# Optimization experiments

Measured on AMD Instinct MI355X. Metric: run time of the kernel, lower is better.

The kernel has to match this reference:

```python
import jax, jax.numpy as jnp
import numpy as np

N_NODES = 50000
N_EDGES = 800000
IN_F, HID, NCLS = 128, 64, 64
N_EXTRA = 2          # layer - 2
K_STEPS = 10
ALPHA = 0.1
BN_EPS = 1e-5


def setup_inputs() -> dict:
    key = jax.random.key(0)
    ks = jax.random.split(key, 20)
    d = {}
    d['x'] = jax.random.normal(ks[0], (N_NODES, IN_F), dtype=jnp.float32)
    d['edge_index'] = jax.random.randint(ks[1], (2, N_EDGES), 0, N_NODES, dtype=jnp.int64)
    s = 1.0 / np.sqrt(HID)
    d['W1'] = jax.random.normal(ks[2], (IN_F, HID), dtype=jnp.float32) / np.sqrt(IN_F)
    d['b1'] = jnp.zeros((HID,), jnp.float32)
    d['W2'] = jax.random.normal(ks[3], (HID, HID), dtype=jnp.float32) * s
    d['b2'] = jnp.zeros((HID,), jnp.float32)
    d['Wx'] = jax.random.normal(ks[4], (N_EXTRA, HID, HID), dtype=jnp.float32) * s
    d['bx'] = jnp.zeros((N_EXTRA, HID), jnp.float32)
    d['g1'] = jnp.ones((HID,), jnp.float32); d['be1'] = jnp.zeros((HID,), jnp.float32)
    d['g2'] = jnp.ones((HID,), jnp.float32); d['be2'] = jnp.zeros((HID,), jnp.float32)
    d['g3'] = jnp.ones((HID,), jnp.float32); d['be3'] = jnp.zeros((HID,), jnp.float32)
    d['Wfc'] = jax.random.normal(ks[5], (HID, NCLS), dtype=jnp.float32) * s
    d['bfc'] = jnp.zeros((NCLS,), jnp.float32)
    return d


def _gcn_norm(edge_index, n):
    # add self-loops, symmetric D^-1/2 (A+I) D^-1/2 normalization (PyG GCNConv default)
    loop = jnp.arange(n, dtype=edge_index.dtype)
    src = jnp.concatenate([edge_index[0], loop])
    dst = jnp.concatenate([edge_index[1], loop])
    deg = jax.ops.segment_sum(jnp.ones(src.shape[0], jnp.float32), dst, num_segments=n)
    dinv = jnp.where(deg > 0, jax.lax.rsqrt(deg), 0.0)
    return src, dst, dinv[src] * dinv[dst]


def _propagate(x, src, dst, w, n):
    # gather-scale-scatter: out[dst] += w * x[src]
    return jax.ops.segment_sum(x[src] * w[:, None], dst, num_segments=n)


def _bn(x, g, b):
    # BatchNorm1d in training mode: batch statistics over the node dim
    m = jnp.mean(x, axis=0)
    v = jnp.var(x, axis=0)
    return g * (x - m) * jax.lax.rsqrt(v + BN_EPS) + b


def reference(x, edge_index, W1, b1, W2, b2, Wx, bx, g1, be1, g2, be2, g3, be3, Wfc, bfc):
    n = x.shape[0]
    src, dst, w = _gcn_norm(edge_index, n)
    h = _propagate(x @ W1, src, dst, w, n) + b1
    h = jax.nn.relu(_bn(h, g1, be1))
    h = _propagate(h @ W2, src, dst, w, n) + b2
    h = jax.nn.relu(_bn(h, g2, be2))
    for i in range(Wx.shape[0]):
        h = _propagate(h @ Wx[i], src, dst, w, n) + bx[i]
        h = jax.nn.relu(_bn(h, g3, be3))
    # APPNP: K power-iteration steps with teleport back to h0
    h0 = h
    for _ in range(K_STEPS):
        h = (1.0 - ALPHA) * _propagate(h, src, dst, w, n) + ALPHA * h0
    out = h @ Wfc + bfc
    return jax.nn.log_softmax(out, axis=1)
```

## Files before the change

### kernel.cpp

```cpp
#include <hip/hip_runtime.h>
#include <hip/hip_fp16.h>
#include <cstdint>
#include <cstddef>

#define NN 50000
#define NE 800000
#define HID 64
#define INF_ 128
#define BN_EPS 1e-5f
#define NGRP (NN / 8)
#define NG16 (NN / 16)
#define SCAN_B 196
#define NSLICE 32

typedef float floatx2 __attribute__((ext_vector_type(2)));

__device__ __forceinline__ float4 h8_to_f4(float2 raw) {
    union { float f; __half2 h; } ua, ub;
    ua.f = raw.x; ub.f = raw.y;
    float2 fa = __half22float2(ua.h), fb = __half22float2(ub.h);
    return make_float4(fa.x, fa.y, fb.x, fb.y);
}
__device__ __forceinline__ float2 f4_to_h8(float4 v) {
    union { float f; __half2 h; } ua, ub;
    ua.h = __float22half2_rn(make_float2(v.x, v.y));
    ub.h = __float22half2_rn(make_float2(v.z, v.w));
    return make_float2(ua.f, ub.f);
}
struct f8 { float v[8]; };
__device__ __forceinline__ f8 h16_to_f8(float4 raw) {
    f8 r;
    union { float f; __half2 h; } u;
    float2 a;
    u.f = raw.x; a = __half22float2(u.h); r.v[0] = a.x; r.v[1] = a.y;
    u.f = raw.y; a = __half22float2(u.h); r.v[2] = a.x; r.v[3] = a.y;
    u.f = raw.z; a = __half22float2(u.h); r.v[4] = a.x; r.v[5] = a.y;
    u.f = raw.w; a = __half22float2(u.h); r.v[6] = a.x; r.v[7] = a.y;
    return r;
}
__device__ __forceinline__ float4 f8_to_h16(const f8& s) {
    union { float f; __half2 h; } u;
    float4 o;
    u.h = __float22half2_rn(make_float2(s.v[0], s.v[1])); o.x = u.f;
    u.h = __float22half2_rn(make_float2(s.v[2], s.v[3])); o.y = u.f;
    u.h = __float22half2_rn(make_float2(s.v[4], s.v[5])); o.z = u.f;
    u.h = __float22half2_rn(make_float2(s.v[6], s.v[7])); o.w = u.f;
    return o;
}

__device__ __forceinline__ void fp8x8_to_f(unsigned lo, unsigned hi, float out[8]) {
    floatx2 a = __builtin_amdgcn_cvt_pk_f32_fp8((int)lo, false);
    floatx2 b = __builtin_amdgcn_cvt_pk_f32_fp8((int)lo, true);
    floatx2 c = __builtin_amdgcn_cvt_pk_f32_fp8((int)hi, false);
    floatx2 d = __builtin_amdgcn_cvt_pk_f32_fp8((int)hi, true);
    out[0] = a[0]; out[1] = a[1]; out[2] = b[0]; out[3] = b[1];
    out[4] = c[0]; out[5] = c[1]; out[6] = d[0]; out[7] = d[1];
}
__device__ __forceinline__ void fp8x16_to_f(uint4 r, float out[16]) {
    fp8x8_to_f(r.x, r.y, out);
    fp8x8_to_f(r.z, r.w, out + 8);
}
__device__ __forceinline__ uint2 f_to_fp8x8(const float v[8]) {
    int w0 = __builtin_amdgcn_cvt_pk_fp8_f32(v[0], v[1], 0, false);
    w0 = __builtin_amdgcn_cvt_pk_fp8_f32(v[2], v[3], w0, true);
    int w1 = __builtin_amdgcn_cvt_pk_fp8_f32(v[4], v[5], 0, false);
    w1 = __builtin_amdgcn_cvt_pk_fp8_f32(v[6], v[7], w1, true);
    uint2 o; o.x = (unsigned)w0; o.y = (unsigned)w1;
    return o;
}
__device__ __forceinline__ uint4 f_to_fp8x16(const float v[16]) {
    uint2 a = f_to_fp8x8(v), b = f_to_fp8x8(v + 8);
    uint4 o; o.x = a.x; o.y = a.y; o.z = b.x; o.w = b.y;
    return o;
}


__global__ void count_k(const int* __restrict__ dst, int* __restrict__ cnt) {
    int e = blockIdx.x * blockDim.x + threadIdx.x;
    if (e < NE) atomicAdd(&cnt[dst[e]], 1);
}

__global__ void dinv_k(const int* __restrict__ cnt, float* __restrict__ dinv) {
    int n = blockIdx.x * blockDim.x + threadIdx.x;
    if (n < NN) dinv[n] = rsqrtf((float)(cnt[n] + 1));
}

__global__ void scan1_k(const int* __restrict__ cnt, int* __restrict__ offs,
                        int* __restrict__ bsum) {
    __shared__ int sh[256];
    int t = threadIdx.x, i = blockIdx.x * 256 + t;
    int v = (i < NN) ? ((cnt[i] + 7) & ~7) : 0;
    sh[t] = v;
    __syncthreads();
    for (int d = 1; d < 256; d <<= 1) {
        int u = (t >= d) ? sh[t - d] : 0;
        __syncthreads();
        sh[t] += u;
        __syncthreads();
    }
    if (i < NN) offs[i] = sh[t] - v;
    if (t == 255) bsum[blockIdx.x] = sh[255];
}

__global__ void scan2_k(const int* __restrict__ bsum, int* __restrict__ bpre,
                        int* __restrict__ offs) {
    __shared__ int sh[256];
    int t = threadIdx.x;
    int v = (t < SCAN_B) ? bsum[t] : 0;
    sh[t] = v;
    __syncthreads();
    for (int d = 1; d < 256; d <<= 1) {
        int u = (t >= d) ? sh[t - d] : 0;
        __syncthreads();
        sh[t] += u;
        __syncthreads();
    }
    bpre[t] = sh[t] - v;
    if (t == 255) offs[NN] = sh[255];
}

__global__ void scan3_k(int* __restrict__ offs, const int* __restrict__ bpre) {
    int i = blockIdx.x * blockDim.x + threadIdx.x;
    if (i < NN) offs[i] += bpre[i >> 8];
}

__global__ void pad_k(const int* __restrict__ cnt, const int* __restrict__ offs,
                      int2* __restrict__ edge2) {
    int n = blockIdx.x * blockDim.x + threadIdx.x;
    if (n >= NN) return;
    int e = offs[n] + cnt[n], e1 = offs[n + 1];
    for (; e < e1; ++e) edge2[e] = make_int2(0, 0);
}

__global__ void scatter_k(const int* __restrict__ src, const int* __restrict__ dst,
                          const int* __restrict__ offs, int* __restrict__ cursor,
                          const float* __restrict__ dinv,
                          int2* __restrict__ edge2) {
    int e = blockIdx.x * blockDim.x + threadIdx.x;
    if (e < NE) {
        int s = src[e], d = dst[e];
        int pos = offs[d] + atomicAdd(&cursor[d], 1);
        edge2[pos] = make_int2(s, __float_as_int(dinv[s] * dinv[d]));
    }
}

template <int K, bool HIN>
__global__ __launch_bounds__(256, 2) void mm_k(const void* __restrict__ Xv,
                                               const float* __restrict__ W,
                                               float2* __restrict__ Y) {
    constexpr int RS = K + 4;
    __shared__ float Xs[64 * RS];
    __shared__ float Ws[K * 64];
    const int t = threadIdx.x;
    const int n0 = blockIdx.x * 64;

    {
        const float4* Wg = (const float4*)W;
        for (int g2 = t; g2 < K * 16; g2 += 256) {
            int row = g2 >> 4, c4 = g2 & 15;
            *(float4*)&Ws[row * 64 + c4 * 4] = Wg[g2];
        }
    }
    if (HIN) {
        const float4* Xg = (const float4*)Xv;
        for (int g2 = t; g2 < 64 * (K / 8); g2 += 256) {
            int row = g2 / (K / 8), c8 = g2 % (K / 8);
            int rr = n0 + row; if (rr >= NN) rr = NN - 1;
            f8 v = h16_to_f8(Xg[(size_t)rr * (K / 8) + c8]);
            float* dp = &Xs[row * RS + c8 * 8];
#pragma unroll
            for (int j = 0; j < 8; ++j) dp[j] = v.v[j];
        }
    } else {
        const float4* Xg = (const float4*)Xv;
        for (int g2 = t; g2 < 64 * (K / 4); g2 += 256) {
            int row = g2 / (K / 4), c4 = g2 % (K / 4);
            int rr = n0 + row; if (rr >= NN) rr = NN - 1;
            *(float4*)&Xs[row * RS + c4 * 4] = Xg[(size_t)rr * (K / 4) + c4];
        }
    }
    __syncthreads();

    const int r0 = (t >> 4) << 2;
    const int c0 = (t & 15) << 2;
    float acc[4][4];
#pragma unroll
    for (int j = 0; j < 4; ++j)
#pragma unroll
        for (int c = 0; c < 4; ++c) acc[j][c] = 0.f;

#pragma unroll 8
    for (int kq = 0; kq < K / 4; ++kq) {
        float4 xv[4];
#pragma unroll
        for (int j = 0; j < 4; ++j)
            xv[j] = *(const float4*)&Xs[(r0 + j) * RS + kq * 4];
        float4 wv[4];
#pragma unroll
        for (int i = 0; i < 4; ++i)
            wv[i] = *(const float4*)&Ws[(kq * 4 + i) * 64 + c0];
#pragma unroll
        for (int j = 0; j < 4; ++j) {
            acc[j][0] = fmaf(xv[j].x, wv[0].x, acc[j][0]);
            acc[j][1] = fmaf(xv[j].x, wv[0].y, acc[j][1]);
            acc[j][2] = fmaf(xv[j].x, wv[0].z, acc[j][2]);
            acc[j][3] = fmaf(xv[j].x, wv[0].w, acc[j][3]);
            acc[j][0] = fmaf(xv[j].y, wv[1].x, acc[j][0]);
            acc[j][1] = fmaf(xv[j].y, wv[1].y, acc[j][1]);
            acc[j][2] = fmaf(xv[j].y, wv[1].z, acc[j][2]);
            acc[j][3] = fmaf(xv[j].y, wv[1].w, acc[j][3]);
            acc[j][0] = fmaf(xv[j].z, wv[2].x, acc[j][0]);
            acc[j][1] = fmaf(xv[j].z, wv[2].y, acc[j][1]);
            acc[j][2] = fmaf(xv[j].z, wv[2].z, acc[j][2]);
            acc[j][3] = fmaf(xv[j].z, wv[2].w, acc[j][3]);
            acc[j][0] = fmaf(xv[j].w, wv[3].x, acc[j][0]);
            acc[j][1] = fmaf(xv[j].w, wv[3].y, acc[j][1]);
            acc[j][2] = fmaf(xv[j].w, wv[3].z, acc[j][2]);
            acc[j][3] = fmaf(xv[j].w, wv[3].w, acc[j][3]);
        }
    }

#pragma unroll
    for (int j = 0; j < 4; ++j) {
        int rr = n0 + r0 + j;
        if (rr < NN)
            Y[(size_t)rr * 16 + (t & 15)] =
                f4_to_h8(make_float4(acc[j][0], acc[j][1], acc[j][2], acc[j][3]));
    }
}

__device__ __forceinline__ void prop_gather8(const float4* __restrict__ X4,
                                             const int2* __restrict__ E,
                                             int e0, int e1, int fl, int slotbase,
                                             float acc[8], float acc2[8]) {
    if (e0 >= e1) return;
    int2 d0 = E[e0 + fl];
    int srcs[8]; float ws[8];
#pragma unroll
    for (int i = 0; i < 8; ++i) {
        srcs[i] = __shfl(d0.x, slotbase + i, 64);
        ws[i]   = __shfl(__int_as_float(d0.y), slotbase + i, 64);
    }
    int2 d1;
    if (e0 + 8 < e1) d1 = E[e0 + 8 + fl];
    float4 rr[8];
#pragma unroll
    for (int i = 0; i < 8; ++i) rr[i] = X4[(size_t)srcs[i] * 8 + fl];

    for (int e = e0; e < e1; ) {
        int en = e + 8;
        float4 rn[8]; float wn[8];
        if (en < e1) {
            int sn[8];
#pragma unroll
            for (int i = 0; i < 8; ++i) {
                sn[i] = __shfl(d1.x, slotbase + i, 64);
                wn[i] = __shfl(__int_as_float(d1.y), slotbase + i, 64);
            }
            if (en + 8 < e1) d1 = E[en + 8 + fl];
#pragma unroll
            for (int i = 0; i < 8; ++i) rn[i] = X4[(size_t)sn[i] * 8 + fl];
        }
        __builtin_amdgcn_sched_barrier(0);
#pragma unroll
        for (int i = 0; i < 8; ++i) {
            f8 x = h16_to_f8(rr[i]);
            float* a = (i & 1) ? acc2 : acc;
#pragma unroll
            for (int j = 0; j < 8; ++j)
                a[j] = fmaf(ws[i], x.v[j], a[j]);
        }
        e = en;
        if (e < e1) {
#pragma unroll
            for (int i = 0; i < 8; ++i) { rr[i] = rn[i]; ws[i] = wn[i]; }
        }
    }
}

__global__ __launch_bounds__(256, 2) void prop_stats_k(
        const float4* __restrict__ X4, const int* __restrict__ offs,
        const int2* __restrict__ edge2, const float* __restrict__ dinv,
        const float* __restrict__ bias, float4* __restrict__ Y4,
        float* __restrict__ stats) {
    const int lane = threadIdx.x & 63;
    const int wave = threadIdx.x >> 6;
    const int slot = lane >> 3;
    const int fl = lane & 7;
    const int slotbase = lane & 56;
    const int wid = blockIdx.x * 4 + wave;
    const int nw = gridDim.x * 4;

    float bias8[8];
    {
        float4 b0 = ((const float4*)bias)[fl * 2];
        float4 b1 = ((const float4*)bias)[fl * 2 + 1];
        bias8[0] = b0.x; bias8[1] = b0.y; bias8[2] = b0.z; bias8[3] = b0.w;
        bias8[4] = b1.x; bias8[5] = b1.y; bias8[6] = b1.z; bias8[7] = b1.w;
    }

    float s1[8], s2[8];
#pragma unroll
    for (int j = 0; j < 8; ++j) { s1[j] = 0.f; s2[j] = 0.f; }

    for (int g = wid; g < NGRP; g += nw) {
        int n = g * 8 + slot;
        float dn = dinv[n];
        float dd = dn * dn;
        f8 self = h16_to_f8(X4[(size_t)n * 8 + fl]);
        float acc[8], acc2[8];
#pragma unroll
        for (int j = 0; j < 8; ++j) { acc[j] = dd * self.v[j]; acc2[j] = 0.f; }
        int e0 = offs[n], e1 = offs[n + 1];
        prop_gather8(X4, edge2, e0, e1, fl, slotbase, acc, acc2);
        f8 o;
#pragma unroll
        for (int j = 0; j < 8; ++j) {
            float a = acc[j] + acc2[j] + bias8[j];
            o.v[j] = a;
            s1[j] += a;
            s2[j] = fmaf(a, a, s2[j]);
        }
        Y4[(size_t)n * 8 + fl] = f8_to_h16(o);
    }

#pragma unroll
    for (int m = 8; m <= 32; m <<= 1) {
#pragma unroll
        for (int j = 0; j < 8; ++j) {
            s1[j] += __shfl_xor(s1[j], m, 64);
            s2[j] += __shfl_xor(s2[j], m, 64);
        }
    }

    __shared__ float red[4][8][16];
    if (lane < 8) {
#pragma unroll
        for (int j = 0; j < 8; ++j) {
            red[wave][lane][j] = s1[j];
            red[wave][lane][8 + j] = s2[j];
        }
    }
    __syncthreads();
    int t = threadIdx.x;
    if (t < 128) {
        int j = t & 63;
        int isq = t >> 6;
        int fli = j >> 3, c = (j & 7) + isq * 8;
        float a = red[0][fli][c] + red[1][fli][c] + red[2][fli][c] + red[3][fli][c];
        atomicAdd(&stats[(blockIdx.x & (NSLICE - 1)) * 128 + isq * 64 + j], a);
    }
}

__global__ __launch_bounds__(256) void bn_relu_k(
        const float4* __restrict__ Y4, const float* __restrict__ slices,
        const float* __restrict__ g, const float* __restrict__ be,
        float4* __restrict__ H4) {
    __shared__ float fs[128];
    int t = threadIdx.x;
    if (t < 128) {
        float s = 0.f;
#pragma unroll
        for (int k = 0; k < NSLICE; ++k) s += slices[k * 128 + t];
        fs[t] = s;
    }
    __syncthreads();
    int i = blockIdx.x * blockDim.x + t;
    if (i >= NN * 8) return;
    int fg = i & 7;
    const float invN = 1.f / (float)NN;
    f8 y = h16_to_f8(Y4[i]);
    float4 gv0 = ((const float4*)g)[fg * 2];
    float4 gv1 = ((const float4*)g)[fg * 2 + 1];
    float4 bv0 = ((const float4*)be)[fg * 2];
    float4 bv1 = ((const float4*)be)[fg * 2 + 1];
    float gv[8] = { gv0.x, gv0.y, gv0.z, gv0.w, gv1.x, gv1.y, gv1.z, gv1.w };
    float bv[8] = { bv0.x, bv0.y, bv0.z, bv0.w, bv1.x, bv1.y, bv1.z, bv1.w };
    f8 o;
#pragma unroll
    for (int j = 0; j < 8; ++j) {
        float m = fs[fg * 8 + j] * invN;
        float v = fs[64 + fg * 8 + j] * invN - m * m;
        float val = fmaf(gv[j] * rsqrtf(v + BN_EPS), y.v[j] - m, bv[j]);
        o.v[j] = val > 0.f ? val : 0.f;
    }
    H4[i] = f8_to_h16(o);
}

__global__ void cvt16to8_k(const float4* __restrict__ H4, uint2* __restrict__ X8) {
    int i = blockIdx.x * blockDim.x + threadIdx.x;
    if (i >= NN * 8) return;
    f8 v = h16_to_f8(H4[i]);
    X8[i] = f_to_fp8x8(v.v);
}

template <bool OUT16>
__global__ __launch_bounds__(256, 2) void appnp8_k(
        const uint4* __restrict__ X8, const float4* __restrict__ H04,
        const int* __restrict__ offs, const int2* __restrict__ edge2,
        const float* __restrict__ dinv,
        uint4* __restrict__ Y8, float4* __restrict__ Y16) {
    const int lane = threadIdx.x & 63;
    const int wave = threadIdx.x >> 6;
    const int slot = lane >> 2;
    const int fl = lane & 3;
    const int quadbase = lane & 60;
    const int wid = blockIdx.x * 4 + wave;
    if (wid >= NG16) return;
    int n = wid * 16 + slot;
    float dn = dinv[n];
    float dd = dn * dn;
    float acc[16];
    {
        float self[16];
        fp8x16_to_f(X8[(size_t)n * 4 + fl], self);
#pragma unroll
        for (int j = 0; j < 16; ++j) acc[j] = dd * self[j];
    }
    int e0 = offs[n], e1 = offs[n + 1];
    if (e0 < e1) {
        int4 d = ((const int4*)(edge2 + e0))[fl];
        int srcs[8]; float ws[8];
#pragma unroll
        for (int k = 0; k < 8; ++k) {
            int sl = quadbase + (k >> 1);
            srcs[k] = __shfl((k & 1) ? d.z : d.x, sl, 64);
            ws[k]   = __shfl(__int_as_float((k & 1) ? d.w : d.y), sl, 64);
        }
        int4 d1;
        if (e0 + 8 < e1) d1 = ((const int4*)(edge2 + e0 + 8))[fl];
        uint4 rr[8];
#pragma unroll
        for (int k = 0; k < 8; ++k) rr[k] = X8[(size_t)srcs[k] * 4 + fl];

        for (int e = e0; e < e1; ) {
            int en = e + 8;
            uint4 rn[8]; float wn[8];
            if (en < e1) {
                int sn[8];
#pragma unroll
                for (int k = 0; k < 8; ++k) {
                    int sl = quadbase + (k >> 1);
                    sn[k] = __shfl((k & 1) ? d1.z : d1.x, sl, 64);
                    wn[k] = __shfl(__int_as_float((k & 1) ? d1.w : d1.y), sl, 64);
                }
                if (en + 8 < e1) d1 = ((const int4*)(edge2 + en + 8))[fl];
#pragma unroll
                for (int k = 0; k < 8; ++k) rn[k] = X8[(size_t)sn[k] * 4 + fl];
            }
            __builtin_amdgcn_sched_barrier(0);
#pragma unroll
            for (int k = 0; k < 8; ++k) {
                float x[16];
                fp8x16_to_f(rr[k], x);
#pragma unroll
                for (int j = 0; j < 16; ++j)
                    acc[j] = fmaf(ws[k], x[j], acc[j]);
            }
            e = en;
            if (e < e1) {
#pragma unroll
                for (int k = 0; k < 8; ++k) { rr[k] = rn[k]; ws[k] = wn[k]; }
            }
        }
    }
    f8 ha = h16_to_f8(H04[(size_t)n * 8 + fl * 2]);
    f8 hb = h16_to_f8(H04[(size_t)n * 8 + fl * 2 + 1]);
    float o[16];
#pragma unroll
    for (int j = 0; j < 8; ++j) {
        o[j] = fmaf(0.9f, acc[j], 0.1f * ha.v[j]);
        o[8 + j] = fmaf(0.9f, acc[8 + j], 0.1f * hb.v[j]);
    }
    if (OUT16) {
        f8 lo, hi;
#pragma unroll
        for (int j = 0; j < 8; ++j) { lo.v[j] = o[j]; hi.v[j] = o[8 + j]; }
        Y16[(size_t)n * 8 + fl * 2] = f8_to_h16(lo);
        Y16[(size_t)n * 8 + fl * 2 + 1] = f8_to_h16(hi);
    } else {
        Y8[(size_t)n * 4 + fl] = f_to_fp8x16(o);
    }
}

__global__ __launch_bounds__(256) void final_k(const float2* __restrict__ H2,
                                               const float* __restrict__ Wfc,
                                               const float* __restrict__ bfc,
                                               float* __restrict__ out) {
    const int t = threadIdx.x;
    const int n0 = blockIdx.x * 64;
    const int r0 = (t >> 4) << 2;
    const int c0 = (t & 15) << 2;

    int r[4];
#pragma unroll
    for (int j = 0; j < 4; ++j) {
        int rr = n0 + r0 + j;
        r[j] = rr < NN ? rr : NN - 1;
    }
    const float2* Xr[4];
#pragma unroll
    for (int j = 0; j < 4; ++j) Xr[j] = H2 + (size_t)r[j] * 16;

    float4 bf = *(const float4*)(bfc + c0);
    float acc[4][4];
#pragma unroll
    for (int j = 0; j < 4; ++j) {
        acc[j][0] = bf.x; acc[j][1] = bf.y; acc[j][2] = bf.z; acc[j][3] = bf.w;
    }

#pragma unroll 4
    for (int kq = 0; kq < 16; ++kq) {
        float4 xv[4];
#pragma unroll
        for (int j = 0; j < 4; ++j) xv[j] = h8_to_f4(Xr[j][kq]);
        float4 wv[4];
#pragma unroll
        for (int i = 0; i < 4; ++i)
            wv[i] = *(const float4*)(Wfc + (size_t)(kq * 4 + i) * 64 + c0);
#pragma unroll
        for (int j = 0; j < 4; ++j) {
            acc[j][0] = fmaf(xv[j].x, wv[0].x, acc[j][0]);
            acc[j][1] = fmaf(xv[j].x, wv[0].y, acc[j][1]);
            acc[j][2] = fmaf(xv[j].x, wv[0].z, acc[j][2]);
            acc[j][3] = fmaf(xv[j].x, wv[0].w, acc[j][3]);
            acc[j][0] = fmaf(xv[j].y, wv[1].x, acc[j][0]);
            acc[j][1] = fmaf(xv[j].y, wv[1].y, acc[j][1]);
            acc[j][2] = fmaf(xv[j].y, wv[1].z, acc[j][2]);
            acc[j][3] = fmaf(xv[j].y, wv[1].w, acc[j][3]);
            acc[j][0] = fmaf(xv[j].z, wv[2].x, acc[j][0]);
            acc[j][1] = fmaf(xv[j].z, wv[2].y, acc[j][1]);
            acc[j][2] = fmaf(xv[j].z, wv[2].z, acc[j][2]);
            acc[j][3] = fmaf(xv[j].z, wv[2].w, acc[j][3]);
            acc[j][0] = fmaf(xv[j].w, wv[3].x, acc[j][0]);
            acc[j][1] = fmaf(xv[j].w, wv[3].y, acc[j][1]);
            acc[j][2] = fmaf(xv[j].w, wv[3].z, acc[j][2]);
            acc[j][3] = fmaf(xv[j].w, wv[3].w, acc[j][3]);
        }
    }

#pragma unroll
    for (int j = 0; j < 4; ++j) {
        float m = fmaxf(fmaxf(acc[j][0], acc[j][1]), fmaxf(acc[j][2], acc[j][3]));
#pragma unroll
        for (int d = 1; d <= 8; d <<= 1) m = fmaxf(m, __shfl_xor(m, d, 64));
        float s = expf(acc[j][0] - m) + expf(acc[j][1] - m) +
                  expf(acc[j][2] - m) + expf(acc[j][3] - m);
#pragma unroll
        for (int d = 1; d <= 8; d <<= 1) s += __shfl_xor(s, d, 64);
        float lse = m + logf(s);
        int rr = n0 + r0 + j;
        if (rr < NN)
            *(float4*)(out + (size_t)rr * 64 + c0) =
                make_float4(acc[j][0] - lse, acc[j][1] - lse,
                            acc[j][2] - lse, acc[j][3] - lse);
    }
}


static inline char* alignup(char* p, size_t a) {
    return (char*)(((uintptr_t)p + a - 1) & ~(uintptr_t)(a - 1));
}

extern "C" void kernel_launch(void* const* d_in, const int* in_sizes, int n_in,
                              void* d_out, int out_size, void* d_ws, size_t ws_size,
                              hipStream_t stream) {
    const float* x   = (const float*)d_in[0];
    const int*   ei  = (const int*)d_in[1];
    const float* W1  = (const float*)d_in[2];
    const float* b1  = (const float*)d_in[3];
    const float* W2  = (const float*)d_in[4];
    const float* b2  = (const float*)d_in[5];
    const float* Wx  = (const float*)d_in[6];
    const float* bx  = (const float*)d_in[7];
    const float* g1  = (const float*)d_in[8];
    const float* be1 = (const float*)d_in[9];
    const float* g2  = (const float*)d_in[10];
    const float* be2 = (const float*)d_in[11];
    const float* g3  = (const float*)d_in[12];
    const float* be3 = (const float*)d_in[13];
    const float* Wfc = (const float*)d_in[14];
    const float* bfc = (const float*)d_in[15];
    float* out = (float*)d_out;

    const int* srcA = ei;
    const int* dstA = ei + NE;

    char* p = (char*)d_ws;
    int*   deg    = (int*)p;   p += NN * 4;
    int*   cursor = (int*)p;   p += NN * 4;
    float* stats  = (float*)p; p += 4 * NSLICE * 128 * 4;
    size_t zbytes = (size_t)(p - (char*)d_ws);
    p = alignup(p, 512);
    int*   offs  = (int*)p;    p += (NN + 4) * 4;   p = alignup(p, 512);
    float* dinv  = (float*)p;  p += NN * 4;         p = alignup(p, 512);
    int*   bsum  = (int*)p;    p += 256 * 4;
    int*   bpre  = (int*)p;    p += 256 * 4;        p = alignup(p, 512);
    int2*  edge2 = (int2*)p;   p += ((size_t)NE + 8 * NN + 256) * 8; p = alignup(p, 512);
    float4* tmpH = (float4*)p; p += (size_t)NN * 64 * 2; p = alignup(p, 512);
    float4* hbH  = (float4*)p; p += (size_t)NN * 64 * 2; p = alignup(p, 512);
    float4* apH  = (float4*)p; p += (size_t)NN * 64 * 2; p = alignup(p, 512);
    float4* pbH  = (float4*)p; p += (size_t)NN * 64 * 2; p = alignup(p, 512);
    uint4*  x8a  = (uint4*)p;  p += (size_t)NN * 64;     p = alignup(p, 512);
    uint4*  x8b  = (uint4*)p;  p += (size_t)NN * 64;

    hipMemsetAsync(d_ws, 0, zbytes, stream);

    count_k<<<(NE + 255) / 256, 256, 0, stream>>>(dstA, deg);
    dinv_k<<<(NN + 255) / 256, 256, 0, stream>>>(deg, dinv);
    scan1_k<<<SCAN_B, 256, 0, stream>>>(deg, offs, bsum);
    scan2_k<<<1, 256, 0, stream>>>(bsum, bpre, offs);
    scan3_k<<<(NN + 255) / 256, 256, 0, stream>>>(offs, bpre);
    pad_k<<<(NN + 255) / 256, 256, 0, stream>>>(deg, offs, edge2);
    scatter_k<<<(NE + 255) / 256, 256, 0, stream>>>(srcA, dstA, offs, cursor, dinv, edge2);

    const int MMG = (NN + 63) / 64;
    const int PG  = (NGRP + 3) / 4;
    const int AG  = (NG16 + 3) / 4;
    const int BNG = (NN * 8 + 255) / 256;
    const int SL  = NSLICE * 128;

    mm_k<INF_, false><<<MMG, 256, 0, stream>>>(x, W1, (float2*)tmpH);
    prop_stats_k<<<PG, 256, 0, stream>>>(tmpH, offs, edge2, dinv, b1, pbH, stats + 0 * SL);
    bn_relu_k<<<BNG, 256, 0, stream>>>(pbH, stats + 0 * SL, g1, be1, hbH);

    mm_k<HID, true><<<MMG, 256, 0, stream>>>(hbH, W2, (float2*)tmpH);
    prop_stats_k<<<PG, 256, 0, stream>>>(tmpH, offs, edge2, dinv, b2, pbH, stats + 1 * SL);
    bn_relu_k<<<BNG, 256, 0, stream>>>(pbH, stats + 1 * SL, g2, be2, hbH);

    for (int L = 0; L < 2; ++L) {
        mm_k<HID, true><<<MMG, 256, 0, stream>>>(hbH, Wx + (size_t)L * 64 * 64, (float2*)tmpH);
        prop_stats_k<<<PG, 256, 0, stream>>>(tmpH, offs, edge2, dinv, bx + (size_t)L * 64,
                                             pbH, stats + (2 + L) * SL);
        bn_relu_k<<<BNG, 256, 0, stream>>>(pbH, stats + (2 + L) * SL, g3, be3, hbH);
    }

    cvt16to8_k<<<BNG, 256, 0, stream>>>(hbH, (uint2*)x8a);
    const uint4* cur8 = x8a;
    for (int it = 0; it < 9; ++it) {
        uint4* o8 = (cur8 == x8a) ? x8b : x8a;
        appnp8_k<false><<<AG, 256, 0, stream>>>(cur8, hbH, offs, edge2, dinv, o8, nullptr);
        cur8 = o8;
    }
    appnp8_k<true><<<AG, 256, 0, stream>>>(cur8, hbH, offs, edge2, dinv, nullptr, apH);

    final_k<<<MMG, 256, 0, stream>>>((const float2*)apH, Wfc, bfc, out);
}
```

Baseline: 500.9 us.

## Sort nodes into degree buckets so waves process similar-degree nodes

Builds a node permutation grouped by in-degree bucket (histogram, scan and scatter kernels) and has the propagation and APPNP kernels process nodes in that order. Each wave's slots then get similar edge counts, which cuts divergence and idle lanes in the gather loops. Also folds the fp16-to-fp8 conversion into the last BN/ReLU kernel, dropping one launch and one pass over memory. The cost is three extra small setup kernels and an indirect perm load per node, and output writes become less coalesced.

Result: no change. 498.9 us (-0.4%).

```diff
diff --git a/kernel.cpp b/kernel.cpp
--- a/kernel.cpp
+++ b/kernel.cpp
@@ -12,6 +12,7 @@
 #define NG16 (NN / 16)
 #define SCAN_B 196
 #define NSLICE 32
+#define NBKT 16
 
 typedef float floatx2 __attribute__((ext_vector_type(2)));
 
@@ -142,6 +143,47 @@
         int pos = offs[d] + atomicAdd(&cursor[d], 1);
         edge2[pos] = make_int2(s, __float_as_int(dinv[s] * dinv[d]));
     }
+}
+
+__global__ void hist_k(const int* __restrict__ cnt, int* __restrict__ hist) {
+    __shared__ int lh[NBKT];
+    int t = threadIdx.x;
+    if (t < NBKT) lh[t] = 0;
+    __syncthreads();
+    int n = blockIdx.x * 256 + t;
+    if (n < NN) {
+        int c = (cnt[n] + 7) >> 3;
+        if (c > NBKT - 1) c = NBKT - 1;
+        atomicAdd(&lh[c], 1);
+    }
+    __syncthreads();
+    if (t < NBKT && lh[t]) atomicAdd(&hist[t], lh[t]);
+}
+
+__global__ void scan16_k(const int* __restrict__ hist, int* __restrict__ bcur) {
+    if (threadIdx.x == 0) {
+        int s = 0;
+        for (int i = 0; i < NBKT; ++i) { bcur[i] = s; s += hist[i]; }
+    }
+}
+
+__global__ void perm_k(const int* __restrict__ cnt, int* __restrict__ bcur,
+                       int* __restrict__ perm) {
+    __shared__ int lh[NBKT], lbase[NBKT];
+    int t = threadIdx.x;
+    if (t < NBKT) lh[t] = 0;
+    __syncthreads();
+    int n = blockIdx.x * 256 + t;
+    int c = 0, r = 0;
+    if (n < NN) {
+        c = (cnt[n] + 7) >> 3;
+        if (c > NBKT - 1) c = NBKT - 1;
+        r = atomicAdd(&lh[c], 1);
+    }
+    __syncthreads();
+    if (t < NBKT) lbase[t] = lh[t] ? atomicAdd(&bcur[t], lh[t]) : 0;
+    __syncthreads();
+    if (n < NN) perm[lbase[c] + r] = n;
 }
 
 template <int K, bool HIN>
@@ -281,8 +323,8 @@
 __global__ __launch_bounds__(256, 2) void prop_stats_k(
         const float4* __restrict__ X4, const int* __restrict__ offs,
         const int2* __restrict__ edge2, const float* __restrict__ dinv,
-        const float* __restrict__ bias, float4* __restrict__ Y4,
-        float* __restrict__ stats) {
+        const float* __restrict__ bias, const int* __restrict__ perm,
+        float4* __restrict__ Y4, float* __restrict__ stats) {
     const int lane = threadIdx.x & 63;
     const int wave = threadIdx.x >> 6;
     const int slot = lane >> 3;
@@ -304,7 +346,7 @@
     for (int j = 0; j < 8; ++j) { s1[j] = 0.f; s2[j] = 0.f; }
 
     for (int g = wid; g < NGRP; g += nw) {
-        int n = g * 8 + slot;
+        int n = perm[g * 8 + slot];
         float dn = dinv[n];
         float dd = dn * dn;
         f8 self = h16_to_f8(X4[(size_t)n * 8 + fl]);
@@ -352,10 +394,11 @@
     }
 }
 
+template <bool EMIT8>
 __global__ __launch_bounds__(256) void bn_relu_k(
         const float4* __restrict__ Y4, const float* __restrict__ slices,
         const float* __restrict__ g, const float* __restrict__ be,
-        float4* __restrict__ H4) {
+        float4* __restrict__ H4, uint2* __restrict__ X8) {
     __shared__ float fs[128];
     int t = threadIdx.x;
     if (t < 128) {
@@ -385,20 +428,14 @@
         o.v[j] = val > 0.f ? val : 0.f;
     }
     H4[i] = f8_to_h16(o);
-}
-
-__global__ void cvt16to8_k(const float4* __restrict__ H4, uint2* __restrict__ X8) {
-    int i = blockIdx.x * blockDim.x + threadIdx.x;
-    if (i >= NN * 8) return;
-    f8 v = h16_to_f8(H4[i]);
-    X8[i] = f_to_fp8x8(v.v);
+    if (EMIT8) X8[i] = f_to_fp8x8(o.v);
 }
 
 template <bool OUT16>
 __global__ __launch_bounds__(256, 2) void appnp8_k(
         const uint4* __restrict__ X8, const float4* __restrict__ H04,
         const int* __restrict__ offs, const int2* __restrict__ edge2,
-        const float* __restrict__ dinv,
+        const float* __restrict__ dinv, const int* __restrict__ perm,
         uint4* __restrict__ Y8, float4* __restrict__ Y16) {
     const int lane = threadIdx.x & 63;
     const int wave = threadIdx.x >> 6;
@@ -407,7 +444,7 @@
     const int quadbase = lane & 60;
     const int wid = blockIdx.x * 4 + wave;
     if (wid >= NG16) return;
-    int n = wid * 16 + slot;
+    int n = perm[wid * 16 + slot];
     float dn = dinv[n];
     float dd = dn * dn;
     float acc[16];
@@ -590,12 +627,15 @@
     int*   deg    = (int*)p;   p += NN * 4;
     int*   cursor = (int*)p;   p += NN * 4;
     float* stats  = (float*)p; p += 4 * NSLICE * 128 * 4;
+    int*   hist   = (int*)p;   p += NBKT * 4;
     size_t zbytes = (size_t)(p - (char*)d_ws);
     p = alignup(p, 512);
     int*   offs  = (int*)p;    p += (NN + 4) * 4;   p = alignup(p, 512);
     float* dinv  = (float*)p;  p += NN * 4;         p = alignup(p, 512);
     int*   bsum  = (int*)p;    p += 256 * 4;
-    int*   bpre  = (int*)p;    p += 256 * 4;        p = alignup(p, 512);
+    int*   bpre  = (int*)p;    p += 256 * 4;
+    int*   bcur  = (int*)p;    p += NBKT * 4;       p = alignup(p, 512);
+    int*   perm  = (int*)p;    p += NN * 4;         p = alignup(p, 512);
     int2*  edge2 = (int2*)p;   p += ((size_t)NE + 8 * NN + 256) * 8; p = alignup(p, 512);
     float4* tmpH = (float4*)p; p += (size_t)NN * 64 * 2; p = alignup(p, 512);
     float4* hbH  = (float4*)p; p += (size_t)NN * 64 * 2; p = alignup(p, 512);
@@ -608,6 +648,9 @@
 
     count_k<<<(NE + 255) / 256, 256, 0, stream>>>(dstA, deg);
     dinv_k<<<(NN + 255) / 256, 256, 0, stream>>>(deg, dinv);
+    hist_k<<<SCAN_B, 256, 0, stream>>>(deg, hist);
+    scan16_k<<<1, 64, 0, stream>>>(hist, bcur);
+    perm_k<<<SCAN_B, 256, 0, stream>>>(deg, bcur, perm);
     scan1_k<<<SCAN_B, 256, 0, stream>>>(deg, offs, bsum);
     scan2_k<<<1, 256, 0, stream>>>(bsum, bpre, offs);
     scan3_k<<<(NN + 255) / 256, 256, 0, stream>>>(offs, bpre);
@@ -621,28 +664,30 @@
     const int SL  = NSLICE * 128;
 
     mm_k<INF_, false><<<MMG, 256, 0, stream>>>(x, W1, (float2*)tmpH);
-    prop_stats_k<<<PG, 256, 0, stream>>>(tmpH, offs, edge2, dinv, b1, pbH, stats + 0 * SL);
-    bn_relu_k<<<BNG, 256, 0, stream>>>(pbH, stats + 0 * SL, g1, be1, hbH);
+    prop_stats_k<<<PG, 256, 0, stream>>>(tmpH, offs, edge2, dinv, b1, perm, pbH, stats + 0 * SL);
+    bn_relu_k<false><<<BNG, 256, 0, stream>>>(pbH, stats + 0 * SL, g1, be1, hbH, nullptr);
 
     mm_k<HID, true><<<MMG, 256, 0, stream>>>(hbH, W2, (float2*)tmpH);
-    prop_stats_k<<<PG, 256, 0, stream>>>(tmpH, offs, edge2, dinv, b2, pbH, stats + 1 * SL);
-    bn_relu_k<<<BNG, 256, 0, stream>>>(pbH, stats + 1 * SL, g2, be2, hbH);
-
-    for (int L = 0; L < 2; ++L) {
-        mm_k<HID, true><<<MMG, 256, 0, stream>>>(hbH, Wx + (size_t)L * 64 * 64, (float2*)tmpH);
-        prop_stats_k<<<PG, 256, 0, stream>>>(tmpH, offs, edge2, dinv, bx + (size_t)L * 64,
-                                             pbH, stats + (2 + L) * SL);
-        bn_relu_k<<<BNG, 256, 0, stream>>>(pbH, stats + (2 + L) * SL, g3, be3, hbH);
-    }
-
-    cvt16to8_k<<<BNG, 256, 0, stream>>>(hbH, (uint2*)x8a);
+    prop_stats_k<<<PG, 256, 0, stream>>>(tmpH, offs, edge2, dinv, b2, perm, pbH, stats + 1 * SL);
+    bn_relu_k<false><<<BNG, 256, 0, stream>>>(pbH, stats + 1 * SL, g2, be2, hbH, nullptr);
+
+    mm_k<HID, true><<<MMG, 256, 0, stream>>>(hbH, Wx + (size_t)0 * 64 * 64, (float2*)tmpH);
+    prop_stats_k<<<PG, 256, 0, stream>>>(tmpH, offs, edge2, dinv, bx + (size_t)0 * 64, perm,
+                                         pbH, stats + 2 * SL);
+    bn_relu_k<false><<<BNG, 256, 0, stream>>>(pbH, stats + 2 * SL, g3, be3, hbH, nullptr);
+
+    mm_k<HID, true><<<MMG, 256, 0, stream>>>(hbH, Wx + (size_t)1 * 64 * 64, (float2*)tmpH);
+    prop_stats_k<<<PG, 256, 0, stream>>>(tmpH, offs, edge2, dinv, bx + (size_t)1 * 64, perm,
+                                         pbH, stats + 3 * SL);
+    bn_relu_k<true><<<BNG, 256, 0, stream>>>(pbH, stats + 3 * SL, g3, be3, hbH, (uint2*)x8a);
+
     const uint4* cur8 = x8a;
     for (int it = 0; it < 9; ++it) {
         uint4* o8 = (cur8 == x8a) ? x8b : x8a;
-        appnp8_k<false><<<AG, 256, 0, stream>>>(cur8, hbH, offs, edge2, dinv, o8, nullptr);
+        appnp8_k<false><<<AG, 256, 0, stream>>>(cur8, hbH, offs, edge2, dinv, perm, o8, nullptr);
         cur8 = o8;
     }
-    appnp8_k<true><<<AG, 256, 0, stream>>>(cur8, hbH, offs, edge2, dinv, nullptr, apH);
+    appnp8_k<true><<<AG, 256, 0, stream>>>(cur8, hbH, offs, edge2, dinv, perm, nullptr, apH);
 
     final_k<<<MMG, 256, 0, stream>>>((const float2*)apH, Wfc, bfc, out);
 }
```
